# Optimization experiments

Hardware: AMD Instinct MI355X
Metric: run time of the kernel (lower is better)

The kernel has to match this reference:

```python
import jax, jax.numpy as jnp
import numpy as np

LAMBDA = 0.5
WINDOW = 2
NUM_SCALES = 2
EPS = 1e-5


def setup_inputs() -> dict:
    key = jax.random.key(0)
    ks = jax.random.split(key, 9)
    N, C, T, Vw = 32, 96, 300, 50
    V = 25
    out_c = 192
    return {
        "x": jax.random.normal(ks[0], (N, C, T, Vw), jnp.float32),
        "xx": jax.random.normal(ks[1], (N, 3, 300, V), jnp.float32),
        "A_res": jax.random.normal(ks[2], (Vw, Vw), jnp.float32) * 1e-6,
        "W": jax.random.normal(ks[3], (out_c, NUM_SCALES * C), jnp.float32) * 0.05,
        "b": jax.random.normal(ks[4], (out_c,), jnp.float32) * 0.01,
        "gamma": jnp.ones((out_c,), jnp.float32),
        "beta": jnp.zeros((out_c,), jnp.float32),
        "running_mean": jax.random.normal(ks[5], (out_c,), jnp.float32) * 0.01,
        "running_var": jax.random.uniform(ks[6], (out_c,), jnp.float32, 0.5, 1.5),
    }


def reference(x, xx, A_res, W, b, gamma, beta, running_mean, running_var):
    # xx: (N, 3, 300, V) -> (N, T=300, V, C=3)
    xxp = jnp.transpose(xx, (0, 2, 3, 1))
    # pairwise squared L2 distances (norm then squared in exp == sum of squares)
    diff = xxp[:, :, :, None, :] - xxp[:, :, None, :, :]      # (N,T,V,V,3)
    dists2 = jnp.sum(diff * diff, axis=-1)                     # (N,T,V,V)
    A_dsg = jnp.exp(-dists2 / LAMBDA)
    # conv3d with (1,1,300,1,1) kernel of 1/300 == mean over the 300 frames
    A_t = jnp.mean(A_dsg, axis=1)                              # (N,V,V)
    # per-sample symmetric normalization D^-1/2 A D^-1/2
    deg = jnp.sum(A_t, axis=-1)                                # (N,V)
    dinv = deg ** -0.5
    A_norm = A_t * dinv[:, :, None] * dinv[:, None, :]
    # kron-style repeat to spatial-temporal graph (N, V*window, V*window)
    A_large = jnp.tile(A_norm, (1, WINDOW, WINDOW))
    A = A_large + A_res                                        # (N,Vw,Vw)
    # conv2d with (1,N,1,1) kernel of 1/N == mean over the batch
    A_scale = jnp.mean(A, axis=0)                              # (Vw,Vw)
    # graph conv
    agg = jnp.einsum('vu,nctu->nctv', A_scale, x)              # (N,C,T,Vw)
    N, C, T, Vw = x.shape
    Vs = Vw // NUM_SCALES
    agg = agg.reshape(N, C, T, NUM_SCALES, Vs)
    agg = jnp.transpose(agg, (0, 3, 1, 2, 4)).reshape(N, NUM_SCALES * C, T, Vs)
    # MLP: 1x1 conv + BN (activation='linear')
    out = jnp.einsum('oc,nctv->notv', W, agg) + b[None, :, None, None]
    scale = gamma * jax.lax.rsqrt(running_var + EPS)
    out = out * scale[None, :, None, None] + (beta - running_mean * scale)[None, :, None, None]
    return jax.nn.relu(out)
```

## Files before the change

### kernel.cpp

```cpp
#include <hip/hip_runtime.h>
#include <hip/hip_bf16.h>

typedef __attribute__((ext_vector_type(8))) short short8;
typedef __attribute__((ext_vector_type(4))) short short4v;
typedef __attribute__((ext_vector_type(4))) float f32x4;
typedef __attribute__((ext_vector_type(2))) float f32x2;
typedef __attribute__((ext_vector_type(2))) unsigned int u32x2;

__device__ __forceinline__ unsigned short f2bf(float f) {
    unsigned int u = __builtin_bit_cast(unsigned int, f);
    u += 0x7fffu + ((u >> 16) & 1u);
    return (unsigned short)(u >> 16);
}
__device__ __forceinline__ unsigned int pack2(float a, float b) {
    union { __hip_bfloat162 h; unsigned int u; } r;
    r.h = __float22bfloat162_rn(make_float2(a, b));
    return r.u;
}
__device__ __forceinline__ short4v cvt4(float a, float b, float c, float d) {
    union { __hip_bfloat162 h[2]; short4v s; } u;
    u.h[0] = __float22bfloat162_rn(make_float2(a, b));
    u.h[1] = __float22bfloat162_rn(make_float2(c, d));
    return u.s;
}

__global__ void kA(const float* __restrict__ xx, float* __restrict__ At_part) {
    __shared__ float xs3[3][60][25];
    const int tc = blockIdx.x, n = blockIdx.y;
    const int tid = threadIdx.x;
    const float* base = xx + (size_t)n * 22500 + tc * 1500;
    for (int idx = tid; idx < 4500; idx += 256) {
        int ch = idx / 1500, rt = idx % 1500;
        xs3[ch][rt / 25][rt % 25] = base[ch * 7500 + rt];
    }
    __syncthreads();
    for (int p = tid; p < 625; p += 256) {
        int v = p / 25, u = p % 25;
        float s = 0.f;
        for (int t = 0; t < 60; ++t) {
            float dx = xs3[0][t][v] - xs3[0][t][u];
            float dy = xs3[1][t][v] - xs3[1][t][u];
            float dz = xs3[2][t][v] - xs3[2][t][u];
            s += __expf(-2.f * (dx * dx + dy * dy + dz * dz));
        }
        At_part[(size_t)(n * 5 + tc) * 625 + p] = s;
    }
}

__global__ void kB1(const float* __restrict__ At_part, float* __restrict__ Acontrib) {
    __shared__ float At[625];
    __shared__ float dinv[25];
    const int n = blockIdx.x, tid = threadIdx.x;
    for (int p = tid; p < 625; p += 256) {
        float s = 0.f;
        for (int tc = 0; tc < 5; ++tc) s += At_part[(size_t)(n * 5 + tc) * 625 + p];
        At[p] = s;
    }
    __syncthreads();
    if (tid < 25) {
        float d = 0.f;
        for (int u = 0; u < 25; ++u) d += At[tid * 25 + u];
        dinv[tid] = rsqrtf(d * (1.f / 300.f));
    }
    __syncthreads();
    for (int p = tid; p < 625; p += 256)
        Acontrib[n * 625 + p] = At[p] * (1.f / 300.f) * dinv[p / 25] * dinv[p % 25] * (1.f / 32.f);
}

__global__ void kB2(const float* __restrict__ Acontrib, const float* __restrict__ A_res,
                    const float* __restrict__ W, const float* __restrict__ b,
                    const float* __restrict__ gamma, const float* __restrict__ beta,
                    const float* __restrict__ rm, const float* __restrict__ rv,
                    short* __restrict__ bsTg, short* __restrict__ Wpg,
                    float* __restrict__ bbg) {
    const int tid = threadIdx.x;
    if (blockIdx.x == 0) {
        __shared__ float macc[625];
        for (int p = tid; p < 625; p += 256) {
            float s = 0.f;
            for (int n = 0; n < 32; ++n) s += Acontrib[n * 625 + p];
            macc[p] = s;
        }
        __syncthreads();
        for (int idx = tid; idx < 64 * 72; idx += 256) {
            int col = idx / 72, u = idx % 72;
            float v = 0.f;
            if (col < 50 && u < 50) v = macc[(col % 25) * 25 + (u % 25)] + A_res[col * 50 + u];
            bsTg[idx] = (short)f2bf(v);
        }
        if (tid < 192) {
            float sc = gamma[tid] * rsqrtf(rv[tid] + 1e-5f);
            bbg[tid] = b[tid] * sc + beta[tid] - rm[tid] * sc;
        }
    } else {
        const int e = (blockIdx.x - 1) * 1024 + tid * 4;
        const int o = e / 192;
        const float sc = gamma[o] * rsqrtf(rv[o] + 1e-5f);
        float4 w = *(const float4*)(W + e);
        short4v s4 = { (short)f2bf(w.x * sc), (short)f2bf(w.y * sc),
                       (short)f2bf(w.z * sc), (short)f2bf(w.w * sc) };
        *(short4v*)(Wpg + e) = s4;
    }
}

__global__ void kB2b(const float* __restrict__ W, const float* __restrict__ gamma,
                     const float* __restrict__ rv, short* __restrict__ Wfrag) {
    const int idx = blockIdx.x * 256 + threadIdx.x;
    const int ot = idx / 384, r = idx - ot * 384;
    const int ks = r / 64, lane = r - ks * 64;
    const int o = ot * 16 + (lane & 15);
    const int k0 = ks * 32 + (lane >> 4) * 8;
    const float sc = gamma[o] * rsqrtf(rv[o] + 1e-5f);
    float4 w0 = *(const float4*)(W + o * 192 + k0);
    float4 w1 = *(const float4*)(W + o * 192 + k0 + 4);
    union { short4v h[2]; short8 v; } u;
    u.h[0] = cvt4(w0.x * sc, w0.y * sc, w0.z * sc, w0.w * sc);
    u.h[1] = cvt4(w1.x * sc, w1.y * sc, w1.z * sc, w1.w * sc);
    *(short8*)(Wfrag + (size_t)idx * 8) = u.v;
}

#define TC1 15
__global__ __launch_bounds__(384, 4)
void kC1(const float* __restrict__ x, const short* __restrict__ bsTg,
         short* __restrict__ agg2) {
    __shared__ __align__(16) char xsb[2 * 12288];
    __shared__ __align__(16) short a2T[2][32][208];

    const int tid = threadIdx.x;
    const int lane = tid & 63;
    const int wid = tid >> 6;
    const int lam = lane & 15;
    const int kc = (lane >> 4) * 8;
    const int cb = (lane >> 4) * 4;
    const int n = blockIdx.y;
    const int t0 = blockIdx.x * TC1;
    const int gb0 = n * 1440000 + t0 * 50;
    const int cgl = wid * 16 + lam;

    short8 af[2][4];
#pragma unroll
    for (int ks = 0; ks < 2; ++ks)
#pragma unroll
        for (int m = 0; m < 4; ++m)
            af[ks][m] = *(const short8*)(bsTg + (m * 16 + lam) * 72 + ks * 32 + kc);

    int goff[7], loff[7];
#pragma unroll
    for (int i = 0; i < 7; ++i) {
        int idx = i * 384 + tid;
        int idc = idx < 2400 ? idx : 2399;
        int c = idc / 25, q = idc - c * 25;
        goff[i] = c * 15000 + 2 * q;
        loff[i] = (c * 128 + q * 4) ^ ((c & 7) << 4);
    }
    int asrc[4];
#pragma unroll
    for (int i = 0; i < 4; ++i) {
        int idx = i * 768 + tid * 2;
        int idc = idx < 2400 ? idx : 2398;
        asrc[i] = idc + (idc / 96) * 8;
    }

    f32x2 pf2[13];
#pragma unroll
    for (int i = 0; i < 13; ++i) {
        int idx = i * 384 + tid;
        idx = idx < 4800 ? idx : 4799;
        int c = idx / 50, q2 = idx - c * 50;
        int tl = q2 >= 25, q = q2 - 25 * tl;
        pf2[i] = *(const f32x2*)(x + gb0 + c * 15000 + tl * 50 + 2 * q);
    }
    for (int idx = tid; idx < 1344; idx += 384) {
        int r = idx / 7, k = idx - r * 7;
        int slot = r / 96, c = r - 96 * slot;
        *(unsigned int*)(xsb + ((slot * 12288 + c * 128 + (50 + 2 * k) * 2) ^ ((c & 7) << 4))) = 0;
    }
#pragma unroll
    for (int i = 0; i < 13; ++i) {
        int idx = i * 384 + tid;
        if (idx < 4800) {
            int c = idx / 50, q2 = idx - c * 50;
            int tl = q2 >= 25, q = q2 - 25 * tl;
            *(unsigned int*)(xsb + ((tl * 12288 + c * 128 + q * 4) ^ ((c & 7) << 4)))
                = pack2(pf2[i].x, pf2[i].y);
        }
    }
    asm volatile("s_waitcnt lgkmcnt(0)" ::: "memory");
    __builtin_amdgcn_s_barrier();

    const f32x4 z = {0.f, 0.f, 0.f, 0.f};
    f32x2 pf[7];

#pragma unroll 1
    for (int tl = 0; tl < TC1; ++tl) {
        const int slot = tl & 1;
        short* a2w = &a2T[slot][0][0];

        if (tl < TC1 - 2) {
            const float* xb2 = x + gb0 + (tl + 2) * 50;
#pragma unroll
            for (int i = 0; i < 7; ++i)
                if (i < 6 || tid < 96) pf[i] = *(const f32x2*)(xb2 + goff[i]);
        }

        short8 xb[2];
#pragma unroll
        for (int ks = 0; ks < 2; ++ks)
            xb[ks] = *(const short8*)(xsb +
                ((slot * 12288 + cgl * 128 + (ks * 32 + kc) * 2) ^ ((cgl & 7) << 4)));
        f32x4 acc1[4];
#pragma unroll
        for (int m = 0; m < 4; ++m) acc1[m] = z;
#pragma unroll
        for (int ks = 0; ks < 2; ++ks)
#pragma unroll
            for (int m = 0; m < 4; ++m)
                acc1[m] = __builtin_amdgcn_mfma_f32_16x16x32_bf16(af[ks][m], xb[ks], acc1[m], 0, 0, 0);

#pragma unroll
        for (int m = 0; m < 3; ++m) {
            short4v sv = cvt4(acc1[m][0], acc1[m][1], acc1[m][2], acc1[m][3]);
#pragma unroll
            for (int r = 0; r < 4; ++r) {
                const int v = m * 16 + cb + r;
                const int s = v >= 25;
                a2w[(v - 25 * s) * 208 + s * 96 + cgl] = sv[r];
            }
        }
        if (cb == 0) {
            a2w[23 * 208 + 96 + cgl] = (short)f2bf(acc1[3][0]);
            a2w[24 * 208 + 96 + cgl] = (short)f2bf(acc1[3][1]);
        }
        asm volatile("s_waitcnt lgkmcnt(0)" ::: "memory");
        __builtin_amdgcn_s_barrier();

        {
            const unsigned int* a2d = (const unsigned int*)a2w;
            unsigned int* dst = (unsigned int*)agg2
                + (size_t)n * 720000 + (size_t)(t0 + tl) * 2400;
#pragma unroll
            for (int i = 0; i < 4; ++i) {
                int idx = i * 768 + tid * 2;
                if (i < 3 || tid < 48) {
                    u32x2 v;
                    v.x = a2d[asrc[i]];
                    v.y = a2d[asrc[i] + 1];
                    *(u32x2*)(dst + idx) = v;
                }
            }
        }

        if (tl < TC1 - 2) {
            char* xw = xsb + slot * 12288;
#pragma unroll
            for (int i = 0; i < 7; ++i)
                if (i < 6 || tid < 96)
                    *(unsigned int*)(xw + loff[i]) = pack2(pf[i].x, pf[i].y);
        }
    }
}

__global__ __launch_bounds__(256, 3)
void kC2(const short* __restrict__ agg2, const short* __restrict__ Wfrag,
         const float* __restrict__ bbg, float* __restrict__ out) {
    __shared__ __align__(16) unsigned int asb[64 * 100];

    const int tid = threadIdx.x;
    const int lane = tid & 63;
    const int wid = tid >> 6;
    const int lam = lane & 15;
    const int kc = (lane >> 4) * 8;
    const int cb = (lane >> 4) * 4;
    const int n = blockIdx.y;
    const int tv0 = blockIdx.x * 64;

    short8 wf[3][6];
    float bb[3];
#pragma unroll
    for (int j = 0; j < 3; ++j) {
        const int ot = wid * 3 + j;
#pragma unroll
        for (int ks = 0; ks < 6; ++ks)
            wf[j][ks] = *(const short8*)(Wfrag + ((size_t)(ot * 6 + ks) * 64 + lane) * 8);
        bb[j] = bbg[ot * 16 + lam];
    }

    {
        const unsigned int* src = (const unsigned int*)agg2 + (size_t)n * 720000;
#pragma unroll
        for (int k = 0; k < 24; ++k) {
            int d = k * 256 + tid;
            int row = d / 96, c2 = d - row * 96;
            int tvg = tv0 + row;
            tvg = tvg < 7500 ? tvg : 7499;
            asb[row * 100 + c2] = src[(size_t)tvg * 96 + c2];
        }
    }
    __syncthreads();

    const f32x4 z = {0.f, 0.f, 0.f, 0.f};
    f32x4 acc[4][3];
#pragma unroll
    for (int m = 0; m < 4; ++m)
#pragma unroll
        for (int j = 0; j < 3; ++j) acc[m][j] = z;

#pragma unroll
    for (int ks = 0; ks < 6; ++ks) {
        short8 a[4];
#pragma unroll
        for (int m = 0; m < 4; ++m)
            a[m] = *(const short8*)((const short*)asb + (m * 16 + lam) * 200 + ks * 32 + kc);
#pragma unroll
        for (int m = 0; m < 4; ++m)
#pragma unroll
            for (int j = 0; j < 3; ++j)
                acc[m][j] = __builtin_amdgcn_mfma_f32_16x16x32_bf16(a[m], wf[j][ks], acc[m][j], 0, 0, 0);
    }

#pragma unroll
    for (int m = 0; m < 4; ++m) {
        const int tvg = tv0 + m * 16 + cb;
        if (tvg < 7500) {
#pragma unroll
            for (int j = 0; j < 3; ++j) {
                const int o = (wid * 3 + j) * 16 + lam;
                float4 v;
                v.x = acc[m][j][0] + bb[j]; v.x = v.x > 0.f ? v.x : 0.f;
                v.y = acc[m][j][1] + bb[j]; v.y = v.y > 0.f ? v.y : 0.f;
                v.z = acc[m][j][2] + bb[j]; v.z = v.z > 0.f ? v.z : 0.f;
                v.w = acc[m][j][3] + bb[j]; v.w = v.w > 0.f ? v.w : 0.f;
                *(float4*)(out + (size_t)(n * 192 + o) * 7500 + tvg) = v;
            }
        }
    }
}

__device__ __forceinline__ void ldx_fb(const float* __restrict__ x, int gbase,
                                       f32x2 (&pf)[7], int tid) {
#pragma unroll
    for (int i = 0; i < 7; ++i) {
        int idx = i * 384 + tid;
        idx = idx < 2400 ? idx : 2399;
        int c = idx / 25, q = idx - c * 25;
        pf[i] = *(const f32x2*)(x + gbase + c * 15000 + 2 * q);
    }
}
__device__ __forceinline__ void stx_fb(char* xsb, int slot, const f32x2 (&pf)[7], int tid) {
#pragma unroll
    for (int i = 0; i < 7; ++i) {
        int idx = i * 384 + tid;
        if (idx < 2400) {
            int c = idx / 25, q = idx - c * 25;
            *(unsigned int*)(xsb + ((slot * 12288 + c * 128 + q * 4) ^ ((c & 7) << 4)))
                = pack2(pf[i].x, pf[i].y);
        }
    }
}

__global__ __launch_bounds__(384, 3)
void kC(const float* __restrict__ x, const short* __restrict__ Wpg,
        const short* __restrict__ bsTg, const float* __restrict__ bbg,
        float* __restrict__ out) {
    __shared__ __align__(16) char xsb[2 * 12288];
    __shared__ __align__(16) short bsT[64 * 72];
    __shared__ __align__(16) short a2T[2][32][208];

    const int tid = threadIdx.x;
    const int lane = tid & 63;
    const int wid = tid >> 6;
    const int lam = lane & 15;
    const int kc = (lane >> 4) * 8;
    const int cb = (lane >> 4) * 4;
    const int n = blockIdx.y;
    const int t0 = blockIdx.x * 4;
    const int gb0 = n * 1440000 + t0 * 50;
    const int cgl = wid * 16 + lam;

    f32x2 pf2[13];
#pragma unroll
    for (int i = 0; i < 13; ++i) {
        int idx = i * 384 + tid;
        idx = idx < 4800 ? idx : 4799;
        int c = idx / 50, q2 = idx - c * 50;
        int tl = q2 >= 25, q = q2 - 25 * tl;
        pf2[i] = *(const f32x2*)(x + gb0 + c * 15000 + tl * 50 + 2 * q);
    }
    short8 wf[2][6];
#pragma unroll
    for (int ot = 0; ot < 2; ++ot)
#pragma unroll
        for (int ks = 0; ks < 6; ++ks)
            wf[ot][ks] = *(const short8*)(Wpg + ((2 * wid + ot) * 16 + lam) * 192 + ks * 32 + kc);
    float bb[2];
#pragma unroll
    for (int ot = 0; ot < 2; ++ot) bb[ot] = bbg[(2 * wid + ot) * 16 + lam];
    {
        const int4* src = (const int4*)bsTg;
        int4* dst = (int4*)bsT;
        for (int i = tid; i < 576; i += 384) dst[i] = src[i];
    }
    for (int idx = tid; idx < 1344; idx += 384) {
        int r = idx / 7, k = idx - r * 7;
        int slot = r / 96, c = r - 96 * slot;
        *(unsigned int*)(xsb + ((slot * 12288 + c * 128 + (50 + 2 * k) * 2) ^ ((c & 7) << 4))) = 0;
    }
    for (int idx = tid; idx < 1456; idx += 384) {
        int buf = idx / 728, rem = idx - buf * 728;
        int row = 25 + rem / 104, col2 = rem - (rem / 104) * 104;
        *((unsigned int*)&a2T[buf][row][0] + col2) = 0;
    }
#pragma unroll
    for (int i = 0; i < 13; ++i) {
        int idx = i * 384 + tid;
        if (idx < 4800) {
            int c = idx / 50, q2 = idx - c * 50;
            int tl = q2 >= 25, q = q2 - 25 * tl;
            *(unsigned int*)(xsb + ((tl * 12288 + c * 128 + q * 4) ^ ((c & 7) << 4)))
                = pack2(pf2[i].x, pf2[i].y);
        }
    }
    asm volatile("s_waitcnt lgkmcnt(0)" ::: "memory");
    __builtin_amdgcn_s_barrier();

    const f32x4 z = {0.f, 0.f, 0.f, 0.f};
    f32x2 pf[7];

#pragma unroll 1
    for (int tl = 0; tl < 4; ++tl) {
        const int slot = tl & 1;
        short* a2w = &a2T[slot][0][0];
        if (tl < 2) ldx_fb(x, gb0 + (tl + 2) * 50, pf, tid);

        short8 xb[2];
#pragma unroll
        for (int ks = 0; ks < 2; ++ks)
            xb[ks] = *(const short8*)(xsb +
                ((slot * 12288 + cgl * 128 + (ks * 32 + kc) * 2) ^ ((cgl & 7) << 4)));
        f32x4 acc1[4];
#pragma unroll
        for (int m = 0; m < 4; ++m) acc1[m] = z;
#pragma unroll
        for (int ks = 0; ks < 2; ++ks)
#pragma unroll
            for (int m = 0; m < 4; ++m) {
                const short8 af = *(const short8*)(bsT + (m * 16 + lam) * 72 + ks * 32 + kc);
                acc1[m] = __builtin_amdgcn_mfma_f32_16x16x32_bf16(af, xb[ks], acc1[m], 0, 0, 0);
            }
#pragma unroll
        for (int m = 0; m < 3; ++m) {
            short4v sv = cvt4(acc1[m][0], acc1[m][1], acc1[m][2], acc1[m][3]);
#pragma unroll
            for (int r = 0; r < 4; ++r) {
                const int v = m * 16 + cb + r;
                const int s = v >= 25;
                a2w[(v - 25 * s) * 208 + s * 96 + cgl] = sv[r];
            }
        }
        if (cb == 0) {
            a2w[23 * 208 + 96 + cgl] = (short)f2bf(acc1[3][0]);
            a2w[24 * 208 + 96 + cgl] = (short)f2bf(acc1[3][1]);
        }
        asm volatile("s_waitcnt lgkmcnt(0)" ::: "memory");
        __builtin_amdgcn_s_barrier();

        f32x4 acc2[2][2];
#pragma unroll
        for (int g = 0; g < 2; ++g) { acc2[g][0] = z; acc2[g][1] = z; }
#pragma unroll
        for (int ks = 0; ks < 6; ++ks) {
            const short8 A0 = *(const short8*)(a2w + lam * 208 + ks * 32 + kc);
            const short8 A1 = *(const short8*)(a2w + (16 + lam) * 208 + ks * 32 + kc);
#pragma unroll
            for (int ot = 0; ot < 2; ++ot) {
                acc2[0][ot] = __builtin_amdgcn_mfma_f32_16x16x32_bf16(A0, wf[ot][ks], acc2[0][ot], 0, 0, 0);
                acc2[1][ot] = __builtin_amdgcn_mfma_f32_16x16x32_bf16(A1, wf[ot][ks], acc2[1][ot], 0, 0, 0);
            }
        }
        if (tl < 2) stx_fb(xsb, slot, pf, tid);

        const int t = t0 + tl;
#pragma unroll
        for (int ot = 0; ot < 2; ++ot) {
            const int o = (2 * wid + ot) * 16 + lam;
            float* op = out + ((size_t)(n * 192 + o) * 300 + t) * 25;
#pragma unroll
            for (int r = 0; r < 4; ++r) {
                float vv = acc2[0][ot][r] + bb[ot];
                op[cb + r] = vv > 0.f ? vv : 0.f;
            }
#pragma unroll
            for (int r = 0; r < 4; ++r) {
                const int tv = 16 + cb + r;
                if (tv < 25) {
                    float vv = acc2[1][ot][r] + bb[ot];
                    op[tv] = vv > 0.f ? vv : 0.f;
                }
            }
        }
    }
}

extern "C" void kernel_launch(void* const* d_in, const int* in_sizes, int n_in,
                              void* d_out, int out_size, void* d_ws, size_t ws_size,
                              hipStream_t stream) {
    const float* x     = (const float*)d_in[0];
    const float* xx    = (const float*)d_in[1];
    const float* A_res = (const float*)d_in[2];
    const float* W     = (const float*)d_in[3];
    const float* b     = (const float*)d_in[4];
    const float* gamma = (const float*)d_in[5];
    const float* beta  = (const float*)d_in[6];
    const float* rm    = (const float*)d_in[7];
    const float* rv    = (const float*)d_in[8];
    float* out = (float*)d_out;

    char* ws = (char*)d_ws;
    float* At_part  = (float*)ws;
    float* Acontrib = (float*)(ws + 400000);
    short* bsTg     = (short*)(ws + 480000);
    short* Wpg      = (short*)(ws + 489216);
    float* bbg      = (float*)(ws + 562944);
    short* Wfrag    = (short*)(ws + 563712);
    short* agg2     = (short*)(ws + 637440);
    const bool bigws = ws_size >= (size_t)637440 + 92160000u;

    kA<<<dim3(5, 32), 256, 0, stream>>>(xx, At_part);
    kB1<<<32, 256, 0, stream>>>(At_part, Acontrib);
    kB2<<<37, 256, 0, stream>>>(Acontrib, A_res, W, b, gamma, beta, rm, rv, bsTg, Wpg, bbg);
    kB2b<<<18, 256, 0, stream>>>(W, gamma, rv, Wfrag);

    if (bigws) {
        kC1<<<dim3(20, 32), 384, 0, stream>>>(x, bsTg, agg2);
        kC2<<<dim3(118, 32), 256, 0, stream>>>(agg2, Wfrag, bbg, out);
    } else {
        kC<<<dim3(75, 32), 384, 0, stream>>>(x, Wpg, bsTg, bbg, out);
    }
}
```

Before: 184.6 us.

## Store kC1 MFMA outputs in fragment-native layout and de-swizzle in kC2

kC1 drops its shared-memory transpose staging and writes each wave's MFMA accumulator fragments straight to global memory as contiguous 16-byte vectors in a fragment-native layout, padded to 64 rows. kC2 reads that padded layout and scatters it into its LDS tile, so each block now handles two time steps (50 rows) and no longer straddles tiles. This removes an LDS round trip and a barrier-protected transpose per time step in kC1, and TC1 drops to 10 with the grid enlarged to match. The cost is a larger intermediate buffer (about 28% more traffic through the padded rows), scalar scattered LDS writes in kC2, and a workspace requirement that may push execution onto the fallback path if the workspace is too small.

```diff
diff --git a/kernel.cpp b/kernel.cpp
--- a/kernel.cpp
+++ b/kernel.cpp
@@ -5,7 +5,6 @@
 typedef __attribute__((ext_vector_type(4))) short short4v;
 typedef __attribute__((ext_vector_type(4))) float f32x4;
 typedef __attribute__((ext_vector_type(2))) float f32x2;
-typedef __attribute__((ext_vector_type(2))) unsigned int u32x2;
 
 __device__ __forceinline__ unsigned short f2bf(float f) {
     unsigned int u = __builtin_bit_cast(unsigned int, f);
@@ -119,12 +118,123 @@
     *(short8*)(Wfrag + (size_t)idx * 8) = u.v;
 }
 
-#define TC1 15
-__global__ __launch_bounds__(384, 4)
+#define TC1 10
+__global__ __launch_bounds__(384, 3)
 void kC1(const float* __restrict__ x, const short* __restrict__ bsTg,
          short* __restrict__ agg2) {
     __shared__ __align__(16) char xsb[2 * 12288];
-    __shared__ __align__(16) short a2T[2][32][208];
+
+    const int tid = threadIdx.x;
+    const int lane = tid & 63;
+    const int wid = tid >> 6;
+    const int lam = lane & 15;
+    const int kc = (lane >> 4) * 8;
+    const int n = blockIdx.y;
+    const int t0 = blockIdx.x * TC1;
+    const int gb0 = n * 1440000 + t0 * 50;
+    const int cgl = wid * 16 + lam;
+
+    short8 af[2][4];
+#pragma unroll
+    for (int ks = 0; ks < 2; ++ks)
+#pragma unroll
+        for (int m = 0; m < 4; ++m)
+            af[ks][m] = *(const short8*)(bsTg + (m * 16 + lam) * 72 + ks * 32 + kc);
+
+    int goff[7], loff[7];
+#pragma unroll
+    for (int i = 0; i < 7; ++i) {
+        int idx = i * 384 + tid;
+        int idc = idx < 2400 ? idx : 2399;
+        int c = idc / 25, q = idc - c * 25;
+        goff[i] = c * 15000 + 2 * q;
+        loff[i] = (c * 128 + q * 4) ^ ((c & 7) << 4);
+    }
+
+    for (int idx = tid; idx < 1344; idx += 384) {
+        int r = idx / 7, k = idx - r * 7;
+        int slot = r / 96, c = r - 96 * slot;
+        *(unsigned int*)(xsb + ((slot * 12288 + c * 128 + (50 + 2 * k) * 2) ^ ((c & 7) << 4))) = 0;
+    }
+
+    f32x2 pf2[13];
+#pragma unroll
+    for (int i = 0; i < 13; ++i) {
+        int idx = i * 384 + tid;
+        idx = idx < 4800 ? idx : 4799;
+        int c = idx / 50, q2 = idx - c * 50;
+        int tl = q2 >= 25, q = q2 - 25 * tl;
+        pf2[i] = *(const f32x2*)(x + gb0 + c * 15000 + tl * 50 + 2 * q);
+    }
+#pragma unroll
+    for (int i = 0; i < 13; ++i) {
+        int idx = i * 384 + tid;
+        if (idx < 4800) {
+            int c = idx / 50, q2 = idx - c * 50;
+            int tl = q2 >= 25, q = q2 - 25 * tl;
+            *(unsigned int*)(xsb + ((tl * 12288 + c * 128 + q * 4) ^ ((c & 7) << 4)))
+                = pack2(pf2[i].x, pf2[i].y);
+        }
+    }
+    asm volatile("s_waitcnt lgkmcnt(0)" ::: "memory");
+    __builtin_amdgcn_s_barrier();
+
+    const f32x4 z = {0.f, 0.f, 0.f, 0.f};
+    f32x2 pf[7];
+    short* aout = agg2 + (((size_t)(n * 300 + t0) * 6 + wid) << 10) + (lane << 4);
+
+#pragma unroll 1
+    for (int tl = 0; tl < TC1; ++tl) {
+        const int slot = tl & 1;
+
+        if (tl < TC1 - 2) {
+            const float* xb2 = x + gb0 + (tl + 2) * 50;
+#pragma unroll
+            for (int i = 0; i < 7; ++i)
+                if (i < 6 || tid < 96) pf[i] = *(const f32x2*)(xb2 + goff[i]);
+        }
+
+        short8 xb[2];
+#pragma unroll
+        for (int ks = 0; ks < 2; ++ks)
+            xb[ks] = *(const short8*)(xsb +
+                ((slot * 12288 + cgl * 128 + (ks * 32 + kc) * 2) ^ ((cgl & 7) << 4)));
+
+        asm volatile("s_waitcnt lgkmcnt(0)" ::: "memory");
+        __builtin_amdgcn_s_barrier();
+
+        f32x4 acc1[4];
+#pragma unroll
+        for (int m = 0; m < 4; ++m) acc1[m] = z;
+#pragma unroll
+        for (int ks = 0; ks < 2; ++ks)
+#pragma unroll
+            for (int m = 0; m < 4; ++m)
+                acc1[m] = __builtin_amdgcn_mfma_f32_16x16x32_bf16(af[ks][m], xb[ks], acc1[m], 0, 0, 0);
+
+        union { short4v h[2]; short8 v; } s0, s1;
+        s0.h[0] = cvt4(acc1[0][0], acc1[0][1], acc1[0][2], acc1[0][3]);
+        s0.h[1] = cvt4(acc1[1][0], acc1[1][1], acc1[1][2], acc1[1][3]);
+        s1.h[0] = cvt4(acc1[2][0], acc1[2][1], acc1[2][2], acc1[2][3]);
+        s1.h[1] = cvt4(acc1[3][0], acc1[3][1], acc1[3][2], acc1[3][3]);
+        short* ap = aout + tl * 6144;
+        *(short8*)(ap) = s0.v;
+        *(short8*)(ap + 8) = s1.v;
+
+        if (tl < TC1 - 2) {
+            char* xw = xsb + slot * 12288;
+#pragma unroll
+            for (int i = 0; i < 7; ++i)
+                if (i < 6 || tid < 96)
+                    *(unsigned int*)(xw + loff[i]) = pack2(pf[i].x, pf[i].y);
+        }
+    }
+}
+
+__global__ __launch_bounds__(256, 3)
+void kC2(const short* __restrict__ agg2, const short* __restrict__ Wfrag,
+         const float* __restrict__ bbg, float* __restrict__ out) {
+    __shared__ __align__(16) short asb[64][200];
 
     const int tid = threadIdx.x;
     const int lane = tid & 63;
@@ -133,146 +243,7 @@
     const int kc = (lane >> 4) * 8;
     const int cb = (lane >> 4) * 4;
     const int n = blockIdx.y;
-    const int t0 = blockIdx.x * TC1;
-    const int gb0 = n * 1440000 + t0 * 50;
-    const int cgl = wid * 16 + lam;
-
-    short8 af[2][4];
-#pragma unroll
-    for (int ks = 0; ks < 2; ++ks)
-#pragma unroll
-        for (int m = 0; m < 4; ++m)
-            af[ks][m] = *(const short8*)(bsTg + (m * 16 + lam) * 72 + ks * 32 + kc);
-
-    int goff[7], loff[7];
-#pragma unroll
-    for (int i = 0; i < 7; ++i) {
-        int idx = i * 384 + tid;
-        int idc = idx < 2400 ? idx : 2399;
-        int c = idc / 25, q = idc - c * 25;
-        goff[i] = c * 15000 + 2 * q;
-        loff[i] = (c * 128 + q * 4) ^ ((c & 7) << 4);
-    }
-    int asrc[4];
-#pragma unroll
-    for (int i = 0; i < 4; ++i) {
-        int idx = i * 768 + tid * 2;
-        int idc = idx < 2400 ? idx : 2398;
-        asrc[i] = idc + (idc / 96) * 8;
-    }
-
-    f32x2 pf2[13];
-#pragma unroll
-    for (int i = 0; i < 13; ++i) {
-        int idx = i * 384 + tid;
-        idx = idx < 4800 ? idx : 4799;
-        int c = idx / 50, q2 = idx - c * 50;
-        int tl = q2 >= 25, q = q2 - 25 * tl;
-        pf2[i] = *(const f32x2*)(x + gb0 + c * 15000 + tl * 50 + 2 * q);
-    }
-    for (int idx = tid; idx < 1344; idx += 384) {
-        int r = idx / 7, k = idx - r * 7;
-        int slot = r / 96, c = r - 96 * slot;
-        *(unsigned int*)(xsb + ((slot * 12288 + c * 128 + (50 + 2 * k) * 2) ^ ((c & 7) << 4))) = 0;
-    }
-#pragma unroll
-    for (int i = 0; i < 13; ++i) {
-        int idx = i * 384 + tid;
-        if (idx < 4800) {
-            int c = idx / 50, q2 = idx - c * 50;
-            int tl = q2 >= 25, q = q2 - 25 * tl;
-            *(unsigned int*)(xsb + ((tl * 12288 + c * 128 + q * 4) ^ ((c & 7) << 4)))
-                = pack2(pf2[i].x, pf2[i].y);
-        }
-    }
-    asm volatile("s_waitcnt lgkmcnt(0)" ::: "memory");
-    __builtin_amdgcn_s_barrier();
-
-    const f32x4 z = {0.f, 0.f, 0.f, 0.f};
-    f32x2 pf[7];
-
-#pragma unroll 1
-    for (int tl = 0; tl < TC1; ++tl) {
-        const int slot = tl & 1;
-        short* a2w = &a2T[slot][0][0];
-
-        if (tl < TC1 - 2) {
-            const float* xb2 = x + gb0 + (tl + 2) * 50;
-#pragma unroll
-            for (int i = 0; i < 7; ++i)
-                if (i < 6 || tid < 96) pf[i] = *(const f32x2*)(xb2 + goff[i]);
-        }
-
-        short8 xb[2];
-#pragma unroll
-        for (int ks = 0; ks < 2; ++ks)
-            xb[ks] = *(const short8*)(xsb +
-                ((slot * 12288 + cgl * 128 + (ks * 32 + kc) * 2) ^ ((cgl & 7) << 4)));
-        f32x4 acc1[4];
-#pragma unroll
-        for (int m = 0; m < 4; ++m) acc1[m] = z;
-#pragma unroll
-        for (int ks = 0; ks < 2; ++ks)
-#pragma unroll
-            for (int m = 0; m < 4; ++m)
-                acc1[m] = __builtin_amdgcn_mfma_f32_16x16x32_bf16(af[ks][m], xb[ks], acc1[m], 0, 0, 0);
-
-#pragma unroll
-        for (int m = 0; m < 3; ++m) {
-            short4v sv = cvt4(acc1[m][0], acc1[m][1], acc1[m][2], acc1[m][3]);
-#pragma unroll
-            for (int r = 0; r < 4; ++r) {
-                const int v = m * 16 + cb + r;
-                const int s = v >= 25;
-                a2w[(v - 25 * s) * 208 + s * 96 + cgl] = sv[r];
-            }
-        }
-        if (cb == 0) {
-            a2w[23 * 208 + 96 + cgl] = (short)f2bf(acc1[3][0]);
-            a2w[24 * 208 + 96 + cgl] = (short)f2bf(acc1[3][1]);
-        }
-        asm volatile("s_waitcnt lgkmcnt(0)" ::: "memory");
-        __builtin_amdgcn_s_barrier();
-
-        {
-            const unsigned int* a2d = (const unsigned int*)a2w;
-            unsigned int* dst = (unsigned int*)agg2
-                + (size_t)n * 720000 + (size_t)(t0 + tl) * 2400;
-#pragma unroll
-            for (int i = 0; i < 4; ++i) {
-                int idx = i * 768 + tid * 2;
-                if (i < 3 || tid < 48) {
-                    u32x2 v;
-                    v.x = a2d[asrc[i]];
-                    v.y = a2d[asrc[i] + 1];
-                    *(u32x2*)(dst + idx) = v;
-                }
-            }
-        }
-
-        if (tl < TC1 - 2) {
-            char* xw = xsb + slot * 12288;
-#pragma unroll
-            for (int i = 0; i < 7; ++i)
-                if (i < 6 || tid < 96)
-                    *(unsigned int*)(xw + loff[i]) = pack2(pf[i].x, pf[i].y);
-        }
-    }
-}
-
-__global__ __launch_bounds__(256, 3)
-void kC2(const short* __restrict__ agg2, const short* __restrict__ Wfrag,
-         const float* __restrict__ bbg, float* __restrict__ out) {
-    __shared__ __align__(16) unsigned int asb[64 * 100];
-
-    const int tid = threadIdx.x;
-    const int lane = tid & 63;
-    const int wid = tid >> 6;
-    const int lam = lane & 15;
-    const int kc = (lane >> 4) * 8;
-    const int cb = (lane >> 4) * 4;
-    const int n = blockIdx.y;
-    const int tv0 = blockIdx.x * 64;
+    const int bx = blockIdx.x;
 
     short8 wf[3][6];
     float bb[3];
@@ -286,14 +257,25 @@
     }
 
     {
-        const unsigned int* src = (const unsigned int*)agg2 + (size_t)n * 720000;
+        const unsigned int* src = (const unsigned int*)agg2
+            + (size_t)(n * 300 + 2 * bx) * 3072;
 #pragma unroll
         for (int k = 0; k < 24; ++k) {
-            int d = k * 256 + tid;
-            int row = d / 96, c2 = d - row * 96;
-            int tvg = tv0 + row;
-            tvg = tvg < 7500 ? tvg : 7499;
-            asb[row * 100 + c2] = src[(size_t)tvg * 96 + c2];
+            int i = k * 256 + tid;
+            unsigned int w = src[i];
+            int tl = i >= 3072;
+            int d = i - tl * 3072;
+            int wid_s = d >> 9, rem = d & 511;
+            int lane_s = rem >> 3, dj = rem & 7;
+            int c = (wid_s << 4) + (lane_s & 15);
+            int v0 = ((dj >> 1) << 4) + ((lane_s >> 4) << 2) + ((dj & 1) << 1);
+            if (v0 < 50) {
+                int s0 = v0 >= 25;
+                asb[tl * 25 + v0 - 25 * s0][s0 * 96 + c] = (short)(w & 0xffffu);
+                int v1 = v0 + 1;
+                int s1 = v1 >= 25;
+                asb[tl * 25 + v1 - 25 * s1][s1 * 96 + c] = (short)(w >> 16);
+            }
         }
     }
     __syncthreads();
@@ -310,7 +292,7 @@
         short8 a[4];
 #pragma unroll
         for (int m = 0; m < 4; ++m)
-            a[m] = *(const short8*)((const short*)asb + (m * 16 + lam) * 200 + ks * 32 + kc);
+            a[m] = *(const short8*)(&asb[m * 16 + lam][ks * 32 + kc]);
 #pragma unroll
         for (int m = 0; m < 4; ++m)
 #pragma unroll
@@ -320,17 +302,22 @@
 
 #pragma unroll
     for (int m = 0; m < 4; ++m) {
-        const int tvg = tv0 + m * 16 + cb;
-        if (tvg < 7500) {
+        const int tvb = m * 16 + cb;
+        if (tvb < 50) {
 #pragma unroll
             for (int j = 0; j < 3; ++j) {
                 const int o = (wid * 3 + j) * 16 + lam;
-                float4 v;
-                v.x = acc[m][j][0] + bb[j]; v.x = v.x > 0.f ? v.x : 0.f;
-                v.y = acc[m][j][1] + bb[j]; v.y = v.y > 0.f ? v.y : 0.f;
-                v.z = acc[m][j][2] + bb[j]; v.z = v.z > 0.f ? v.z : 0.f;
-                v.w = acc[m][j][3] + bb[j]; v.w = v.w > 0.f ? v.w : 0.f;
-                *(float4*)(out + (size_t)(n * 192 + o) * 7500 + tvg) = v;
+                float* op = out + (size_t)(n * 192 + o) * 7500 + bx * 50 + tvb;
+                float v0 = acc[m][j][0] + bb[j]; v0 = v0 > 0.f ? v0 : 0.f;
+                float v1 = acc[m][j][1] + bb[j]; v1 = v1 > 0.f ? v1 : 0.f;
+                f32x2 p0 = {v0, v1};
+                *(f32x2*)op = p0;
+                if (tvb < 48) {
+                    float v2 = acc[m][j][2] + bb[j]; v2 = v2 > 0.f ? v2 : 0.f;
+                    float v3 = acc[m][j][3] + bb[j]; v3 = v3 > 0.f ? v3 : 0.f;
+                    f32x2 p1 = {v2, v3};
+                    *(f32x2*)(op + 2) = p1;
+                }
             }
         }
     }
@@ -523,7 +510,7 @@
     float* bbg      = (float*)(ws + 562944);
     short* Wfrag    = (short*)(ws + 563712);
     short* agg2     = (short*)(ws + 637440);
-    const bool bigws = ws_size >= (size_t)637440 + 92160000u;
+    const bool bigws = ws_size >= (size_t)637440 + 117964800u;
 
     kA<<<dim3(5, 32), 256, 0, stream>>>(xx, At_part);
     kB1<<<32, 256, 0, stream>>>(At_part, Acontrib);
@@ -531,8 +518,8 @@
     kB2b<<<18, 256, 0, stream>>>(W, gamma, rv, Wfrag);
 
     if (bigws) {
-        kC1<<<dim3(20, 32), 384, 0, stream>>>(x, bsTg, agg2);
-        kC2<<<dim3(118, 32), 256, 0, stream>>>(agg2, Wfrag, bbg, out);
+        kC1<<<dim3(30, 32), 384, 0, stream>>>(x, bsTg, agg2);
+        kC2<<<dim3(150, 32), 256, 0, stream>>>(agg2, Wfrag, bbg, out);
     } else {
         kC<<<dim3(75, 32), 384, 0, stream>>>(x, Wpg, bsTg, bbg, out);
     }
```

Result: slower. 236.6 us (+28.1%).
